# Kernel tuning notes

Measured on AMD Instinct MI355X. Metric: run time of the kernel, lower is better.

## Reference

```python
import jax, jax.numpy as jnp
import numpy as np

EPS = 1e-5
N_HEAD = 16


def layernorm(x, g, b):
    mu = jnp.mean(x, axis=-1, keepdims=True)
    var = jnp.mean(jnp.square(x - mu), axis=-1, keepdims=True)
    return (x - mu) * jax.lax.rsqrt(var + EPS) * g + b


def setup_inputs() -> dict:
    key = jax.random.key(0)
    ks = jax.random.split(key, 8)
    B, S, D = 4, 2048, 1024
    F = 4 * D
    s = 0.02
    return {
        "h": jax.random.normal(ks[0], (B, S, D), jnp.float32),
        "ln1_g": jnp.ones((D,), jnp.float32),
        "ln1_b": jnp.zeros((D,), jnp.float32),
        "wq": jax.random.normal(ks[1], (D, D), jnp.float32) * s,
        "bq": jnp.zeros((D,), jnp.float32),
        "wk": jax.random.normal(ks[2], (D, D), jnp.float32) * s,
        "bk": jnp.zeros((D,), jnp.float32),
        "wv": jax.random.normal(ks[3], (D, D), jnp.float32) * s,
        "bv": jnp.zeros((D,), jnp.float32),
        "wo": jax.random.normal(ks[4], (D, D), jnp.float32) * s,
        "bo": jnp.zeros((D,), jnp.float32),
        "ln2_g": jnp.ones((D,), jnp.float32),
        "ln2_b": jnp.zeros((D,), jnp.float32),
        "wfc": jax.random.normal(ks[5], (F, D), jnp.float32) * s,
        "bfc": jnp.zeros((F,), jnp.float32),
        "wproj": jax.random.normal(ks[6], (D, F), jnp.float32) * s,
        "bproj": jnp.zeros((D,), jnp.float32),
    }


def reference(h, ln1_g, ln1_b, wq, bq, wk, bk, wv, bv, wo, bo,
              ln2_g, ln2_b, wfc, bfc, wproj, bproj):
    B, S, D = h.shape
    H = N_HEAD
    Dh = D // H

    # --- attention sub-block ---
    r = h
    x = layernorm(h, ln1_g, ln1_b)
    q = (x @ wq.T + bq).reshape(B, S, H, Dh)
    k = (x @ wk.T + bk).reshape(B, S, H, Dh)
    v = (x @ wv.T + bv).reshape(B, S, H, Dh)

    scores = jnp.einsum("bqhd,bkhd->bhqk", q, k) / jnp.sqrt(jnp.float32(Dh))
    causal = jnp.tril(jnp.ones((S, S), bool))  # [S,S]
    scores = jnp.where(causal, scores, jnp.finfo(scores.dtype).min)
    probs = jax.nn.softmax(scores, axis=-1)
    o = jnp.einsum("bhqk,bkhd->bqhd", probs, v).reshape(B, S, D)
    h = r + (o @ wo.T + bo)

    # --- MLP sub-block ---
    r = h
    x = layernorm(h, ln2_g, ln2_b)
    x = jax.nn.gelu(x @ wfc.T + bfc, approximate=True)  # NewGELU (tanh)
    h = r + (x @ wproj.T + bproj)
    return h
```

## Files before the change

kernel.cpp:

```cpp
#include <hip/hip_runtime.h>
#include <hip/hip_bf16.h>
#include <stdint.h>


typedef short bf16x8 __attribute__((ext_vector_type(8)));
typedef float f32x4  __attribute__((ext_vector_type(4)));
typedef float f32x16 __attribute__((ext_vector_type(16)));
typedef short s16x4  __attribute__((ext_vector_type(4)));

__device__ __forceinline__ short f2bf(float f) {
  union { float f; uint32_t u; } a;
  a.f = f;
  uint32_t r = a.u + 0x7fffu + ((a.u >> 16) & 1u);
  return (short)(r >> 16);
}

__device__ __forceinline__ unsigned cvt_pk_bf16(float lo, float hi_) {
  unsigned r;
  asm("v_cvt_pk_bf16_f32 %0, %1, %2" : "=v"(r) : "v"(lo), "v"(hi_));
  return r;
}

__device__ __forceinline__ void gload_lds16(const void* g, void* l) {
  __builtin_amdgcn_global_load_lds(
      (const __attribute__((address_space(1))) void*)g,
      (__attribute__((address_space(3))) void*)l, 16, 0, 0);
}

__device__ __forceinline__ float gelu_f(float x) {
  float y = 0.7978845608028654f * (x + 0.044715f * x * x * x);
  y = fminf(fmaxf(y, -20.f), 20.f);
  float e = __expf(2.f * y);
  return 0.5f * x * (1.f + (e - 1.f) / (e + 1.f));
}

__global__ __launch_bounds__(256)
void cvt_f32_bf16(const float* __restrict__ in, short* __restrict__ out, int n4) {
  int i = blockIdx.x * 256 + threadIdx.x;
  if (i < n4) {
    float4 v = ((const float4*)in)[i];
    s16x4 o;
    o[0] = f2bf(v.x); o[1] = f2bf(v.y); o[2] = f2bf(v.z); o[3] = f2bf(v.w);
    ((s16x4*)out)[i] = o;
  }
}

__global__ __launch_bounds__(256)
void ln_fwd(const float* __restrict__ x, const float* __restrict__ g,
            const float* __restrict__ b, short* __restrict__ y) {
  const long row = blockIdx.x;
  const int t = threadIdx.x;
  const float4 xv = ((const float4*)(x + row * 1024))[t];
  float s  = xv.x + xv.y + xv.z + xv.w;
  float ss = xv.x * xv.x + xv.y * xv.y + xv.z * xv.z + xv.w * xv.w;
#pragma unroll
  for (int m = 1; m < 64; m <<= 1) {
    s  += __shfl_xor(s, m);
    ss += __shfl_xor(ss, m);
  }
  __shared__ float rs[4], rss[4];
  const int wid = t >> 6, lane = t & 63;
  if (lane == 0) { rs[wid] = s; rss[wid] = ss; }
  __syncthreads();
  s  = rs[0] + rs[1] + rs[2] + rs[3];
  ss = rss[0] + rss[1] + rss[2] + rss[3];
  const float mu   = s * (1.f / 1024.f);
  const float var  = ss * (1.f / 1024.f) - mu * mu;
  const float rstd = rsqrtf(var + 1e-5f);
  const float4 gv = ((const float4*)g)[t];
  const float4 bv = ((const float4*)b)[t];
  s16x4 ov;
  ov[0] = f2bf((xv.x - mu) * rstd * gv.x + bv.x);
  ov[1] = f2bf((xv.y - mu) * rstd * gv.y + bv.y);
  ov[2] = f2bf((xv.z - mu) * rstd * gv.z + bv.z);
  ov[3] = f2bf((xv.w - mu) * rstd * gv.w + bv.w);
  *(s16x4*)(y + row * 1024 + t * 4) = ov;
}

template <int OUT_BF16, int HAS_RES, int HAS_GELU>
__global__ __launch_bounds__(512, 1)
void gemm_bt4(const short* __restrict__ A, const short* __restrict__ W,
              const float* __restrict__ bias, const float* __restrict__ res,
              void* __restrict__ out, int M, int N, int K) {
  __shared__ short As[3][128 * 64];
  __shared__ short Bs[3][256 * 64];
  const int tid = threadIdx.x;
  const int wid = tid >> 6, lane = tid & 63;
  const int l16 = lane & 15, lg = lane >> 4;
  const int wm = wid >> 2, wn = wid & 3;

  const int nbx = N >> 8;
  const int nwg = nbx * (M >> 7);
  int flat = (int)blockIdx.x;
  if ((nwg & 7) == 0) flat = (flat & 7) * (nwg >> 3) + (flat >> 3);
  const int brow = (flat / nbx) * 128, bcol = (flat % nbx) * 256;

  f32x4 acc[4][4] = {};

  const int r0 = tid >> 3, g0 = tid & 7;

  auto STAGE_A = [&](int buf, int kt) {
#pragma unroll
    for (int i = 0; i < 2; ++i) {
      const int row = i * 64 + r0;
      gload_lds16(A + (long)(brow + row) * K + kt + 8 * (g0 ^ (row & 7)),
                  &As[buf][(i * 512 + tid) * 8]);
    }
  };
  auto STAGE_B = [&](int buf, int kt, int i) {
    const int row = i * 64 + r0;
    gload_lds16(W + (long)(bcol + row) * K + kt + 8 * (g0 ^ (row & 7)),
                &Bs[buf][(i * 512 + tid) * 8]);
  };

  int ra[4], rb[4];
#pragma unroll
  for (int m = 0; m < 4; ++m) ra[m] = wm * 64 + m * 16 + l16;
#pragma unroll
  for (int n = 0; n < 4; ++n) rb[n] = wn * 64 + n * 16 + l16;

  const int NT = K >> 6;
  STAGE_A(0, 0); STAGE_B(0, 0, 0); STAGE_B(0, 0, 1); STAGE_B(0, 0, 2); STAGE_B(0, 0, 3);
  STAGE_A(1, 64); STAGE_B(1, 64, 0); STAGE_B(1, 64, 1); STAGE_B(1, 64, 2); STAGE_B(1, 64, 3);
  asm volatile("s_waitcnt vmcnt(6)" ::: "memory");
  __builtin_amdgcn_s_barrier();

  int cur = 0;
  for (int t = 0; t < NT; ++t) {
    const bool st = (t + 2 < NT);
    int sb = cur + 2; if (sb >= 3) sb -= 3;
    const int kt2 = (t + 2) << 6;

    bf16x8 af[4], bf[4];
#pragma unroll
    for (int m = 0; m < 4; ++m)
      af[m] = *(const bf16x8*)&As[cur][ra[m] * 64 + 8 * (lg ^ (ra[m] & 7))];
#pragma unroll
    for (int n = 0; n < 4; ++n)
      bf[n] = *(const bf16x8*)&Bs[cur][rb[n] * 64 + 8 * (lg ^ (rb[n] & 7))];
    if (st) { STAGE_A(sb, kt2); STAGE_B(sb, kt2, 0); }
    __builtin_amdgcn_s_barrier();
    asm volatile("s_waitcnt lgkmcnt(0)" ::: "memory");
    __builtin_amdgcn_sched_barrier(0);
    __builtin_amdgcn_s_setprio(1);
#pragma unroll
    for (int m = 0; m < 4; ++m)
#pragma unroll
      for (int n = 0; n < 4; ++n)
        acc[m][n] = __builtin_amdgcn_mfma_f32_16x16x32_bf16(af[m], bf[n], acc[m][n], 0, 0, 0);
    __builtin_amdgcn_s_setprio(0);
    __builtin_amdgcn_s_barrier();

#pragma unroll
    for (int m = 0; m < 4; ++m)
      af[m] = *(const bf16x8*)&As[cur][ra[m] * 64 + 8 * ((4 + lg) ^ (ra[m] & 7))];
#pragma unroll
    for (int n = 0; n < 4; ++n)
      bf[n] = *(const bf16x8*)&Bs[cur][rb[n] * 64 + 8 * ((4 + lg) ^ (rb[n] & 7))];
    if (st) { STAGE_B(sb, kt2, 1); STAGE_B(sb, kt2, 2); STAGE_B(sb, kt2, 3); }
    __builtin_amdgcn_s_barrier();
    asm volatile("s_waitcnt lgkmcnt(0)" ::: "memory");
    __builtin_amdgcn_sched_barrier(0);
    __builtin_amdgcn_s_setprio(1);
#pragma unroll
    for (int m = 0; m < 4; ++m)
#pragma unroll
      for (int n = 0; n < 4; ++n)
        acc[m][n] = __builtin_amdgcn_mfma_f32_16x16x32_bf16(af[m], bf[n], acc[m][n], 0, 0, 0);
    __builtin_amdgcn_s_setprio(0);
    if (t + 2 < NT)      asm volatile("s_waitcnt vmcnt(6)" ::: "memory");
    else if (t + 1 < NT) asm volatile("s_waitcnt vmcnt(0)" ::: "memory");
    __builtin_amdgcn_s_barrier();

    cur = (cur + 1 == 3) ? 0 : cur + 1;
  }

#pragma unroll
  for (int n = 0; n < 4; ++n) {
    const int col = bcol + wn * 64 + n * 16 + l16;
    const float bb = bias[col];
#pragma unroll
    for (int m = 0; m < 4; ++m) {
#pragma unroll
      for (int j = 0; j < 4; ++j) {
        const long row = brow + wm * 64 + m * 16 + lg * 4 + j;
        float vv = acc[m][n][j] + bb;
        if (HAS_GELU) vv = gelu_f(vv);
        if (HAS_RES) vv += res[row * N + col];
        if (OUT_BF16) ((short*)out)[row * N + col] = f2bf(vv);
        else          ((float*)out)[row * N + col] = vv;
      }
    }
  }
}

__global__ __launch_bounds__(256)
void transpose_v(const short* __restrict__ v, short* __restrict__ vtg,
                 int S, int ldv, int H) {
  __shared__ short t[64][66];
  const int bh = blockIdx.y, b = bh / H, hh = bh % H;
  const int s0 = blockIdx.x * 64;
  const int tid = threadIdx.x;
#pragma unroll
  for (int i = 0; i < 2; ++i) {
    const int c = i * 256 + tid;
    const int sl = c >> 3, d8 = (c & 7) * 8;
    bf16x8 vv = *(const bf16x8*)&v[((long)b * S + s0 + sl) * ldv + hh * 64 + d8];
#pragma unroll
    for (int j = 0; j < 8; ++j) t[d8 + j][sl] = vv[j];
  }
  __syncthreads();
#pragma unroll
  for (int i = 0; i < 2; ++i) {
    const int c = i * 256 + tid;
    const int dl = c >> 3, s8 = (c & 7) * 8;
    bf16x8 ov;
#pragma unroll
    for (int j = 0; j < 8; ++j) ov[j] = t[dl][s8 + j];
    *(bf16x8*)&vtg[((long)bh * 64 + dl) * S + s0 + s8] = ov;
  }
}

__global__ __launch_bounds__(256, 4)
void attn_fwd2(const short* __restrict__ qg, const short* __restrict__ kg,
               const short* __restrict__ vtg, short* __restrict__ og,
               int S, int ldq, int D, int H) {
  const int tid = threadIdx.x, wid = tid >> 6, lane = tid & 63;
  const int l31 = lane & 31, hi = lane >> 5;
  const int fid = blockIdx.x;
  const int bh = fid & 63;
  const int b = bh / H, hh = bh % H;
  static const int perm[16] = {15, 0, 8, 7, 1, 14, 6, 9, 13, 2, 10, 5, 3, 12, 4, 11};
  const int qt = perm[(fid >> 6) & 15];
  const int q0 = qt * 128;
  const long qbase = (long)b * S * ldq + hh * 64;
  const long obase = (long)b * S * D + hh * 64;
  const long vbase = (long)bh * 64 * S;

  __shared__ short Ks[2][64 * 64];
  __shared__ short Vs[2][64 * 64];

  auto STAGE = [&](int buf, int k0) {
#pragma unroll
    for (int i = 0; i < 2; ++i) {
      const int c = i * 256 + tid;
      const int row = c >> 3, gl = c & 7;
      gload_lds16(&kg[qbase + (long)(k0 + row) * ldq + 8 * (gl ^ (row & 7))],
                  &Ks[buf][(i * 256 + wid * 64) * 8]);
      gload_lds16(&vtg[vbase + (long)row * S + k0 + 8 * (gl ^ (row & 7))],
                  &Vs[buf][(i * 256 + wid * 64) * 8]);
    }
  };

  const float kScale = 0.125f * 1.44269504089f;

  const int qw = q0 + wid * 32;
  const int qv = qw + l31;

  bf16x8 qf[4];
#pragma unroll
  for (int s = 0; s < 4; ++s)
    qf[s] = *(const bf16x8*)&qg[qbase + (long)qv * ldq + 16 * s + 8 * hi];

  f32x16 oa[2] = {};
  float mr = -3000.f, lr = 0.f;

  const int ntiles = qt * 2 + 2;

  STAGE(0, 0);
  for (int t = 0; t < ntiles; ++t) {
    const int cur = t & 1;
    const int k0 = t * 64;
    if (t + 1 < ntiles) {
      STAGE(cur ^ 1, k0 + 64);
      asm volatile("s_waitcnt vmcnt(4)" ::: "memory");
    } else {
      asm volatile("s_waitcnt vmcnt(0)" ::: "memory");
    }
    __builtin_amdgcn_s_barrier();

    if (k0 < qw + 32) {
      f32x16 st[2] = {};
#pragma unroll
      for (int s = 0; s < 4; ++s) {
        const int g = ((s << 1) | hi) ^ (l31 & 7);
        bf16x8 kf0 = *(const bf16x8*)&Ks[cur][l31 * 64 + 8 * g];
        bf16x8 kf1 = *(const bf16x8*)&Ks[cur][(32 + l31) * 64 + 8 * g];
        st[0] = __builtin_amdgcn_mfma_f32_32x32x16_bf16(kf0, qf[s], st[0], 0, 0, 0);
        st[1] = __builtin_amdgcn_mfma_f32_32x32x16_bf16(kf1, qf[s], st[1], 0, 0, 0);
      }

      const bool need_mask = (k0 + 63 > qw);
      float pv[2][16];
#pragma unroll
      for (int kb = 0; kb < 2; ++kb)
#pragma unroll
        for (int r = 0; r < 16; ++r) {
          float v = st[kb][r] * kScale;
          if (need_mask) {
            const int key = k0 + kb * 32 + (r & 3) + 8 * (r >> 2) + 4 * hi;
            if (key > qv) v = -1e30f;
          }
          pv[kb][r] = v;
        }

      float t8[8];
#pragma unroll
      for (int j = 0; j < 8; ++j)
        t8[j] = fmaxf(fmaxf(pv[0][j], pv[0][8 + j]), fmaxf(pv[1][j], pv[1][8 + j]));
      float rm = fmaxf(fmaxf(fmaxf(t8[0], t8[1]), fmaxf(t8[2], t8[3])),
                       fmaxf(fmaxf(t8[4], t8[5]), fmaxf(t8[6], t8[7])));
      rm = fmaxf(rm, __shfl_xor(rm, 32));

      const bool defer = (bool)__all(rm <= mr + 8.f);
      const float mn = defer ? mr : fmaxf(mr, rm);

      float a0 = 0.f, a1 = 0.f, a2 = 0.f, a3 = 0.f;
#pragma unroll
      for (int r = 0; r < 8; ++r) {
        float p0 = exp2f(pv[0][r] - mn);      pv[0][r] = p0;      a0 += p0;
        float p1 = exp2f(pv[0][8 + r] - mn);  pv[0][8 + r] = p1;  a1 += p1;
        float p2 = exp2f(pv[1][r] - mn);      pv[1][r] = p2;      a2 += p2;
        float p3 = exp2f(pv[1][8 + r] - mn);  pv[1][8 + r] = p3;  a3 += p3;
      }
      float ls = (a0 + a1) + (a2 + a3);
      ls += __shfl_xor(ls, 32);

      if (!defer) {
        const float alpha = exp2f(mr - mn);
        lr = lr * alpha + ls;
        mr = mn;
#pragma unroll
        for (int r = 0; r < 16; ++r) {
          const int crow = (r & 3) + 8 * (r >> 2) + 4 * hi;
          const float ar = __shfl(alpha, crow | (lane & 32));
          oa[0][r] *= ar;
          oa[1][r] *= ar;
        }
      } else {
        lr += ls;
      }

      bf16x8 pa[4];
#pragma unroll
      for (int kb = 0; kb < 2; ++kb) {
        unsigned pk[8], ex[8];
#pragma unroll
        for (int i2 = 0; i2 < 8; ++i2)
          pk[i2] = cvt_pk_bf16(pv[kb][2 * i2], pv[kb][2 * i2 + 1]);
#pragma unroll
        for (int i2 = 0; i2 < 8; ++i2)
          ex[i2] = (unsigned)__shfl_xor((int)pk[i2], 32);
        union { unsigned u[4]; bf16x8 v8; } f0, f1;
        f0.u[0] = hi ? ex[2] : pk[0];
        f0.u[1] = hi ? ex[3] : pk[1];
        f0.u[2] = hi ? pk[2] : ex[0];
        f0.u[3] = hi ? pk[3] : ex[1];
        f1.u[0] = hi ? ex[6] : pk[4];
        f1.u[1] = hi ? ex[7] : pk[5];
        f1.u[2] = hi ? pk[6] : ex[4];
        f1.u[3] = hi ? pk[7] : ex[5];
        pa[2 * kb]     = f0.v8;
        pa[2 * kb + 1] = f1.v8;
      }

#pragma unroll
      for (int s = 0; s < 4; ++s) {
        const int g = ((s << 1) | hi) ^ (l31 & 7);
        bf16x8 vf0 = *(const bf16x8*)&Vs[cur][l31 * 64 + 8 * g];
        bf16x8 vf1 = *(const bf16x8*)&Vs[cur][(32 + l31) * 64 + 8 * g];
        oa[0] = __builtin_amdgcn_mfma_f32_32x32x16_bf16(pa[s], vf0, oa[0], 0, 0, 0);
        oa[1] = __builtin_amdgcn_mfma_f32_32x32x16_bf16(pa[s], vf1, oa[1], 0, 0, 0);
      }
    }

    asm volatile("s_waitcnt lgkmcnt(0)" ::: "memory");
    __builtin_amdgcn_s_barrier();
  }

  const float linv = 1.f / lr;
#pragma unroll
  for (int r = 0; r < 16; ++r) {
    const int crow = (r & 3) + 8 * (r >> 2) + 4 * hi;
    const float li = __shfl(linv, crow | (lane & 32));
    const long row = qw + crow;
    og[obase + row * D + l31]      = f2bf(oa[0][r] * li);
    og[obase + row * D + 32 + l31] = f2bf(oa[1][r] * li);
  }
}

extern "C" void kernel_launch(void* const* d_in, const int* in_sizes, int n_in,
                              void* d_out, int out_size, void* d_ws, size_t ws_size,
                              hipStream_t stream) {
  (void)in_sizes; (void)n_in; (void)out_size; (void)ws_size;
  const float* h     = (const float*)d_in[0];
  const float* ln1_g = (const float*)d_in[1];
  const float* ln1_b = (const float*)d_in[2];
  const float* wq    = (const float*)d_in[3];
  const float* bq    = (const float*)d_in[4];
  const float* wk    = (const float*)d_in[5];
  const float* bk    = (const float*)d_in[6];
  const float* wv    = (const float*)d_in[7];
  const float* bv    = (const float*)d_in[8];
  const float* wo    = (const float*)d_in[9];
  const float* bo    = (const float*)d_in[10];
  const float* ln2_g = (const float*)d_in[11];
  const float* ln2_b = (const float*)d_in[12];
  const float* wfc   = (const float*)d_in[13];
  const float* bfc   = (const float*)d_in[14];
  const float* wproj = (const float*)d_in[15];
  const float* bproj = (const float*)d_in[16];

  const int B = 4, S = 2048, D = 1024, H = 16, F = 4096, T = B * S;
  const int D3 = 3 * D;

  char* ws = (char*)d_ws;
  size_t off = 0;
  auto alloc = [&](size_t bytes) {
    void* p = ws + off;
    off += (bytes + 255) & ~(size_t)255;
    return p;
  };
  short* xb   = (short*)alloc((size_t)T * D * 2);
  short* qkv  = (short*)alloc((size_t)T * D3 * 2);
  short* ob   = (short*)alloc((size_t)T * D * 2);
  float* h2   = (float*)alloc((size_t)T * D * 4);
  short* wqkvb  = (short*)alloc((size_t)D3 * D * 2);
  short* wob    = (short*)alloc((size_t)D * D * 2);
  short* wfcb   = (short*)alloc((size_t)F * D * 2);
  short* wprojb = (short*)alloc((size_t)D * F * 2);
  float* bqkv   = (float*)alloc((size_t)D3 * 4);
  short* ub  = qkv;
  short* vtg = (short*)h2;

  cvt_f32_bf16<<<dim3(D * D / 4 / 256), 256, 0, stream>>>(wq, wqkvb, D * D / 4);
  cvt_f32_bf16<<<dim3(D * D / 4 / 256), 256, 0, stream>>>(wk, wqkvb + (size_t)D * D, D * D / 4);
  cvt_f32_bf16<<<dim3(D * D / 4 / 256), 256, 0, stream>>>(wv, wqkvb + (size_t)2 * D * D, D * D / 4);
  cvt_f32_bf16<<<dim3(D * D / 4 / 256), 256, 0, stream>>>(wo, wob, D * D / 4);
  cvt_f32_bf16<<<dim3(F * D / 4 / 256), 256, 0, stream>>>(wfc, wfcb, F * D / 4);
  cvt_f32_bf16<<<dim3(D * F / 4 / 256), 256, 0, stream>>>(wproj, wprojb, D * F / 4);
  hipMemcpyAsync(bqkv,         bq, D * 4, hipMemcpyDeviceToDevice, stream);
  hipMemcpyAsync(bqkv + D,     bk, D * 4, hipMemcpyDeviceToDevice, stream);
  hipMemcpyAsync(bqkv + 2 * D, bv, D * 4, hipMemcpyDeviceToDevice, stream);

  ln_fwd<<<dim3(T), 256, 0, stream>>>(h, ln1_g, ln1_b, xb);
  gemm_bt4<1, 0, 0><<<dim3((T / 128) * (D3 / 256)), 512, 0, stream>>>(
      xb, wqkvb, bqkv, nullptr, qkv, T, D3, D);
  transpose_v<<<dim3(S / 64, B * H), 256, 0, stream>>>(qkv + 2 * D, vtg, S, D3, H);
  attn_fwd2<<<dim3((S / 128) * (B * H / 64) * 64), 256, 0, stream>>>(
      qkv, qkv + D, vtg, ob, S, D3, D, H);
  gemm_bt4<0, 1, 0><<<dim3((T / 128) * (D / 256)), 512, 0, stream>>>(
      ob, wob, bo, h, h2, T, D, D);

  ln_fwd<<<dim3(T), 256, 0, stream>>>(h2, ln2_g, ln2_b, xb);
  gemm_bt4<1, 0, 1><<<dim3((T / 128) * (F / 256)), 512, 0, stream>>>(
      xb, wfcb, bfc, nullptr, ub, T, F, D);
  gemm_bt4<0, 1, 0><<<dim3((T / 128) * (D / 256)), 512, 0, stream>>>(
      ub, wprojb, bproj, h2, (float*)d_out, T, D, F);
}
```

Measured before the change: 401.6 us.

## Enlarge GEMM tiles to 256x256 with double-buffered staggered A/B staging

Replaces the 128x256 triple-buffered GEMM with a 256x256-tile kernel. Each wave now holds a 128x64 accumulator block, and the loads are restructured so B is staged two k-steps ahead while A is staged one step ahead, each in halves across four MFMA phases. The larger tile doubles the reuse of each B fragment and cuts global/LDS traffic per flop. In exchange it uses more accumulator registers and halves the number of workgroups, which hurts wave fill on the small-N GEMMs (T=8192, N=1024 gives only 128 blocks on a 256-CU part).

Result: slower. 452.9 us (+12.8%).

```diff
diff --git a/kernel.cpp b/kernel.cpp
--- a/kernel.cpp
+++ b/kernel.cpp
@@ -79,66 +79,74 @@
 
 template <int OUT_BF16, int HAS_RES, int HAS_GELU>
 __global__ __launch_bounds__(512, 1)
-void gemm_bt4(const short* __restrict__ A, const short* __restrict__ W,
-              const float* __restrict__ bias, const float* __restrict__ res,
-              void* __restrict__ out, int M, int N, int K) {
-  __shared__ short As[3][128 * 64];
-  __shared__ short Bs[3][256 * 64];
+void gemm256(const short* __restrict__ A, const short* __restrict__ W,
+             const float* __restrict__ bias, const float* __restrict__ res,
+             void* __restrict__ out, int M, int N, int K) {
+  __shared__ short As[2][256 * 64];
+  __shared__ short Bs[2][256 * 64];
   const int tid = threadIdx.x;
   const int wid = tid >> 6, lane = tid & 63;
   const int l16 = lane & 15, lg = lane >> 4;
   const int wm = wid >> 2, wn = wid & 3;
 
   const int nbx = N >> 8;
-  const int nwg = nbx * (M >> 7);
+  const int nwg = nbx * (M >> 8);
   int flat = (int)blockIdx.x;
   if ((nwg & 7) == 0) flat = (flat & 7) * (nwg >> 3) + (flat >> 3);
-  const int brow = (flat / nbx) * 128, bcol = (flat % nbx) * 256;
-
-  f32x4 acc[4][4] = {};
+  const int brow = (flat / nbx) * 256, bcol = (flat % nbx) * 256;
+
+  f32x4 acc[2][4][4] = {};
 
   const int r0 = tid >> 3, g0 = tid & 7;
 
-  auto STAGE_A = [&](int buf, int kt) {
+  auto STAGE_A = [&](int buf, int half, int kt) {
 #pragma unroll
     for (int i = 0; i < 2; ++i) {
-      const int row = i * 64 + r0;
+      const int row = half * 128 + i * 64 + r0;
       gload_lds16(A + (long)(brow + row) * K + kt + 8 * (g0 ^ (row & 7)),
-                  &As[buf][(i * 512 + tid) * 8]);
+                  &As[buf][(half * 1024 + i * 512 + tid) * 8]);
     }
   };
-  auto STAGE_B = [&](int buf, int kt, int i) {
-    const int row = i * 64 + r0;
-    gload_lds16(W + (long)(bcol + row) * K + kt + 8 * (g0 ^ (row & 7)),
-                &Bs[buf][(i * 512 + tid) * 8]);
+  auto STAGE_B = [&](int buf, int half, int kt) {
+#pragma unroll
+    for (int i = 0; i < 2; ++i) {
+      const int row = half * 128 + i * 64 + r0;
+      gload_lds16(W + (long)(bcol + row) * K + kt + 8 * (g0 ^ (row & 7)),
+                  &Bs[buf][(half * 1024 + i * 512 + tid) * 8]);
+    }
   };
 
-  int ra[4], rb[4];
-#pragma unroll
-  for (int m = 0; m < 4; ++m) ra[m] = wm * 64 + m * 16 + l16;
+  int ra0[4], ra1[4], rb[4];
+#pragma unroll
+  for (int m = 0; m < 4; ++m) {
+    ra0[m] = wm * 128 + m * 16 + l16;
+    ra1[m] = wm * 128 + 64 + m * 16 + l16;
+  }
 #pragma unroll
   for (int n = 0; n < 4; ++n) rb[n] = wn * 64 + n * 16 + l16;
 
   const int NT = K >> 6;
-  STAGE_A(0, 0); STAGE_B(0, 0, 0); STAGE_B(0, 0, 1); STAGE_B(0, 0, 2); STAGE_B(0, 0, 3);
-  STAGE_A(1, 64); STAGE_B(1, 64, 0); STAGE_B(1, 64, 1); STAGE_B(1, 64, 2); STAGE_B(1, 64, 3);
-  asm volatile("s_waitcnt vmcnt(6)" ::: "memory");
+  STAGE_A(0, 0, 0); STAGE_A(0, 1, 0); STAGE_B(0, 0, 0); STAGE_B(0, 1, 0);
+  STAGE_B(1, 0, 64); STAGE_B(1, 1, 64);
+  asm volatile("s_waitcnt vmcnt(4)" ::: "memory");
   __builtin_amdgcn_s_barrier();
 
-  int cur = 0;
   for (int t = 0; t < NT; ++t) {
-    const bool st = (t + 2 < NT);
-    int sb = cur + 2; if (sb >= 3) sb -= 3;
-    const int kt2 = (t + 2) << 6;
-
-    bf16x8 af[4], bf[4];
-#pragma unroll
-    for (int m = 0; m < 4; ++m)
-      af[m] = *(const bf16x8*)&As[cur][ra[m] * 64 + 8 * (lg ^ (ra[m] & 7))];
-#pragma unroll
-    for (int n = 0; n < 4; ++n)
-      bf[n] = *(const bf16x8*)&Bs[cur][rb[n] * 64 + 8 * (lg ^ (rb[n] & 7))];
-    if (st) { STAGE_A(sb, kt2); STAGE_B(sb, kt2, 0); }
+    const int c = t & 1;
+    const bool st1 = (t + 1 < NT), st2 = (t + 2 < NT);
+    const int kt1 = (t + 1) << 6, kt2 = (t + 2) << 6;
+
+    bf16x8 b0[4], b1[4], a[4];
+
+#pragma unroll
+    for (int n = 0; n < 4; ++n) {
+      b0[n] = *(const bf16x8*)&Bs[c][rb[n] * 64 + 8 * (lg ^ (rb[n] & 7))];
+      b1[n] = *(const bf16x8*)&Bs[c][rb[n] * 64 + 8 * ((4 + lg) ^ (rb[n] & 7))];
+    }
+#pragma unroll
+    for (int m = 0; m < 4; ++m)
+      a[m] = *(const bf16x8*)&As[c][ra0[m] * 64 + 8 * (lg ^ (ra0[m] & 7))];
+    if (st1) STAGE_A(c ^ 1, 0, kt1);
     __builtin_amdgcn_s_barrier();
     asm volatile("s_waitcnt lgkmcnt(0)" ::: "memory");
     __builtin_amdgcn_sched_barrier(0);
@@ -147,17 +155,14 @@
     for (int m = 0; m < 4; ++m)
 #pragma unroll
       for (int n = 0; n < 4; ++n)
-        acc[m][n] = __builtin_amdgcn_mfma_f32_16x16x32_bf16(af[m], bf[n], acc[m][n], 0, 0, 0);
+        acc[0][m][n] = __builtin_amdgcn_mfma_f32_16x16x32_bf16(a[m], b0[n], acc[0][m][n], 0, 0, 0);
     __builtin_amdgcn_s_setprio(0);
     __builtin_amdgcn_s_barrier();
 
 #pragma unroll
     for (int m = 0; m < 4; ++m)
-      af[m] = *(const bf16x8*)&As[cur][ra[m] * 64 + 8 * ((4 + lg) ^ (ra[m] & 7))];
-#pragma unroll
-    for (int n = 0; n < 4; ++n)
-      bf[n] = *(const bf16x8*)&Bs[cur][rb[n] * 64 + 8 * ((4 + lg) ^ (rb[n] & 7))];
-    if (st) { STAGE_B(sb, kt2, 1); STAGE_B(sb, kt2, 2); STAGE_B(sb, kt2, 3); }
+      a[m] = *(const bf16x8*)&As[c][ra1[m] * 64 + 8 * (lg ^ (ra1[m] & 7))];
+    if (st1) STAGE_A(c ^ 1, 1, kt1);
     __builtin_amdgcn_s_barrier();
     asm volatile("s_waitcnt lgkmcnt(0)" ::: "memory");
     __builtin_amdgcn_sched_barrier(0);
@@ -166,13 +171,44 @@
     for (int m = 0; m < 4; ++m)
 #pragma unroll
       for (int n = 0; n < 4; ++n)
-        acc[m][n] = __builtin_amdgcn_mfma_f32_16x16x32_bf16(af[m], bf[n], acc[m][n], 0, 0, 0);
+        acc[1][m][n] = __builtin_amdgcn_mfma_f32_16x16x32_bf16(a[m], b0[n], acc[1][m][n], 0, 0, 0);
     __builtin_amdgcn_s_setprio(0);
-    if (t + 2 < NT)      asm volatile("s_waitcnt vmcnt(6)" ::: "memory");
-    else if (t + 1 < NT) asm volatile("s_waitcnt vmcnt(0)" ::: "memory");
-    __builtin_amdgcn_s_barrier();
-
-    cur = (cur + 1 == 3) ? 0 : cur + 1;
+    __builtin_amdgcn_s_barrier();
+
+#pragma unroll
+    for (int m = 0; m < 4; ++m)
+      a[m] = *(const bf16x8*)&As[c][ra0[m] * 64 + 8 * ((4 + lg) ^ (ra0[m] & 7))];
+    if (st2) STAGE_B(c, 0, kt2);
+    __builtin_amdgcn_s_barrier();
+    asm volatile("s_waitcnt lgkmcnt(0)" ::: "memory");
+    __builtin_amdgcn_sched_barrier(0);
+    __builtin_amdgcn_s_setprio(1);
+#pragma unroll
+    for (int m = 0; m < 4; ++m)
+#pragma unroll
+      for (int n = 0; n < 4; ++n)
+        acc[0][m][n] = __builtin_amdgcn_mfma_f32_16x16x32_bf16(a[m], b1[n], acc[0][m][n], 0, 0, 0);
+    __builtin_amdgcn_s_setprio(0);
+    __builtin_amdgcn_s_barrier();
+
+#pragma unroll
+    for (int m = 0; m < 4; ++m)
+      a[m] = *(const bf16x8*)&As[c][ra1[m] * 64 + 8 * ((4 + lg) ^ (ra1[m] & 7))];
+    if (st2) STAGE_B(c, 1, kt2);
+    __builtin_amdgcn_s_barrier();
+    asm volatile("s_waitcnt lgkmcnt(0)" ::: "memory");
+    __builtin_amdgcn_sched_barrier(0);
+    __builtin_amdgcn_s_setprio(1);
+#pragma unroll
+    for (int m = 0; m < 4; ++m)
+#pragma unroll
+      for (int n = 0; n < 4; ++n)
+        acc[1][m][n] = __builtin_amdgcn_mfma_f32_16x16x32_bf16(a[m], b1[n], acc[1][m][n], 0, 0, 0);
+    __builtin_amdgcn_s_setprio(0);
+
+    if (st2)      asm volatile("s_waitcnt vmcnt(4)" ::: "memory");
+    else if (st1) asm volatile("s_waitcnt vmcnt(0)" ::: "memory");
+    __builtin_amdgcn_s_barrier();
   }
 
 #pragma unroll
@@ -180,15 +216,18 @@
     const int col = bcol + wn * 64 + n * 16 + l16;
     const float bb = bias[col];
 #pragma unroll
-    for (int m = 0; m < 4; ++m) {
-#pragma unroll
-      for (int j = 0; j < 4; ++j) {
-        const long row = brow + wm * 64 + m * 16 + lg * 4 + j;
-        float vv = acc[m][n][j] + bb;
-        if (HAS_GELU) vv = gelu_f(vv);
-        if (HAS_RES) vv += res[row * N + col];
-        if (OUT_BF16) ((short*)out)[row * N + col] = f2bf(vv);
-        else          ((float*)out)[row * N + col] = vv;
+    for (int mh = 0; mh < 2; ++mh) {
+#pragma unroll
+      for (int m = 0; m < 4; ++m) {
+#pragma unroll
+        for (int j = 0; j < 4; ++j) {
+          const long row = brow + wm * 128 + mh * 64 + m * 16 + lg * 4 + j;
+          float vv = acc[mh][m][n][j] + bb;
+          if (HAS_GELU) vv = gelu_f(vv);
+          if (HAS_RES) vv += res[row * N + col];
+          if (OUT_BF16) ((short*)out)[row * N + col] = f2bf(vv);
+          else          ((float*)out)[row * N + col] = vv;
+        }
       }
     }
   }
@@ -444,17 +483,17 @@
   hipMemcpyAsync(bqkv + 2 * D, bv, D * 4, hipMemcpyDeviceToDevice, stream);
 
   ln_fwd<<<dim3(T), 256, 0, stream>>>(h, ln1_g, ln1_b, xb);
-  gemm_bt4<1, 0, 0><<<dim3((T / 128) * (D3 / 256)), 512, 0, stream>>>(
+  gemm256<1, 0, 0><<<dim3((T / 256) * (D3 / 256)), 512, 0, stream>>>(
       xb, wqkvb, bqkv, nullptr, qkv, T, D3, D);
   transpose_v<<<dim3(S / 64, B * H), 256, 0, stream>>>(qkv + 2 * D, vtg, S, D3, H);
   attn_fwd2<<<dim3((S / 128) * (B * H / 64) * 64), 256, 0, stream>>>(
       qkv, qkv + D, vtg, ob, S, D3, D, H);
-  gemm_bt4<0, 1, 0><<<dim3((T / 128) * (D / 256)), 512, 0, stream>>>(
+  gemm256<0, 1, 0><<<dim3((T / 256) * (D / 256)), 512, 0, stream>>>(
       ob, wob, bo, h, h2, T, D, D);
 
   ln_fwd<<<dim3(T), 256, 0, stream>>>(h2, ln2_g, ln2_b, xb);
-  gemm_bt4<1, 0, 1><<<dim3((T / 128) * (F / 256)), 512, 0, stream>>>(
+  gemm256<1, 0, 1><<<dim3((T / 256) * (F / 256)), 512, 0, stream>>>(
       xb, wfcb, bfc, nullptr, ub, T, F, D);
-  gemm_bt4<0, 1, 0><<<dim3((T / 128) * (D / 256)), 512, 0, stream>>>(
+  gemm256<0, 1, 0><<<dim3((T / 256) * (D / 256)), 512, 0, stream>>>(
       ub, wprojb, bproj, h2, (float*)d_out, T, D, F);
 }
```
